# Kernel optimization log

Hardware: AMD Instinct MI355X
Metric: run time of the kernel (lower is better)

The kernel has to match this reference:

```python
import jax, jax.numpy as jnp
import numpy as np

D_MODEL = 1024
N_HEADS = 16
D_HEAD = D_MODEL // N_HEADS
IGNORE = -100000.0


def setup_inputs() -> dict:
    key = jax.random.key(0)
    ks = jax.random.split(key, 12)
    B, S = 4, 2048
    x_q = jax.random.normal(ks[0], (B, S, D_MODEL), dtype=jnp.float32)
    x_kv = jax.random.normal(ks[1], (B, S, D_MODEL), dtype=jnp.float32)
    # mask[q, k] == True means the score is replaced with IGNORE (masked out)
    mask = jax.random.randint(ks[2], (S, S), 0, 2) == 1
    sq = 1.0 / np.sqrt(D_MODEL)
    sh = 1.0 / np.sqrt(D_HEAD)
    W_Q = jax.random.normal(ks[3], (N_HEADS, D_MODEL, D_HEAD), dtype=jnp.float32) * sq
    W_K = jax.random.normal(ks[4], (N_HEADS, D_MODEL, D_HEAD), dtype=jnp.float32) * sq
    W_V = jax.random.normal(ks[5], (N_HEADS, D_MODEL, D_HEAD), dtype=jnp.float32) * sq
    W_O = jax.random.normal(ks[6], (N_HEADS, D_HEAD, D_MODEL), dtype=jnp.float32) * sh
    b_Q = jnp.zeros((N_HEADS, D_HEAD), dtype=jnp.float32)
    b_K = jnp.zeros((N_HEADS, D_HEAD), dtype=jnp.float32)
    b_V = jnp.zeros((N_HEADS, D_HEAD), dtype=jnp.float32)
    b_O = jnp.zeros((D_MODEL,), dtype=jnp.float32)
    return {"x_q": x_q, "x_kv": x_kv, "mask": mask,
            "W_Q": W_Q, "W_K": W_K, "W_V": W_V, "W_O": W_O,
            "b_Q": b_Q, "b_K": b_K, "b_V": b_V, "b_O": b_O}


def reference(x_q, x_kv, mask, W_Q, W_K, W_V, W_O, b_Q, b_K, b_V, b_O):
    # per-head QKV projections: b s d, n d h -> b s n h
    q = jnp.einsum('bsd,ndh->bsnh', x_q, W_Q) + b_Q
    k = jnp.einsum('bsd,ndh->bsnh', x_kv, W_K) + b_K
    v = jnp.einsum('bsd,ndh->bsnh', x_kv, W_V) + b_V
    scale = 1.0 / np.sqrt(D_HEAD)  # flex_attention default scaling
    # scores: [B, H, Sq, Sk]
    scores = jnp.einsum('bqnh,bknh->bnqk', q, k) * scale
    # score_mod: where mask True -> IGNORE
    scores = jnp.where(mask[None, None, :, :], jnp.float32(IGNORE), scores)
    attn = jax.nn.softmax(scores, axis=-1)
    z = jnp.einsum('bnqk,bknh->bqnh', attn, v)  # [B, Sq, H, Dh]
    # per-head output projection then sum over heads
    out = jnp.einsum('bqnh,nhd->bqd', z, W_O) + b_O
    return (out, z)
```

## Files before the change

kernel.cpp:

```cpp
#include <hip/hip_runtime.h>

#define S_LEN 2048
#define NHEAD 16
#define DHEAD 64
#define DMODEL 1024
#define BATCH 4
#define SC2 0.18033688011112042f

typedef short bf16x8 __attribute__((ext_vector_type(8)));
typedef float f32x4 __attribute__((ext_vector_type(4)));
typedef unsigned short u16;
typedef unsigned short u16x8 __attribute__((ext_vector_type(8)));
typedef unsigned short u16x4 __attribute__((ext_vector_type(4)));
typedef unsigned long long u64;
typedef unsigned long long u64x2 __attribute__((ext_vector_type(2)));

__device__ __forceinline__ u16 f2b(float f) {
  unsigned u = __builtin_bit_cast(unsigned, f);
  u += 0x7FFFu + ((u >> 16) & 1u);
  return (u16)(u >> 16);
}
__device__ __forceinline__ float b2f(u16 v) {
  unsigned u = ((unsigned)v) << 16;
  return __builtin_bit_cast(float, u);
}
__device__ __forceinline__ f32x4 mfma16(bf16x8 a, bf16x8 b, f32x4 c) {
  return __builtin_amdgcn_mfma_f32_16x16x32_bf16(a, b, c, 0, 0, 0);
}
__device__ __forceinline__ void load_lds16(const void* g, void* l) {
  __builtin_amdgcn_global_load_lds(
      (const __attribute__((address_space(1))) unsigned int*)g,
      (__attribute__((address_space(3))) unsigned int*)l, 16, 0, 0);
}
__device__ __forceinline__ void fexp2x4(float& a, float& b, float& c, float& d) {
  asm("v_exp_f32 %0, %0\n\t"
      "v_exp_f32 %1, %1\n\t"
      "v_exp_f32 %2, %2\n\t"
      "v_exp_f32 %3, %3\n\t"
      "s_nop 1"
      : "+v"(a), "+v"(b), "+v"(c), "+v"(d));
}
__device__ __forceinline__ unsigned cvtpk(float lo, float hi) {
  unsigned r;
  asm("v_cvt_pk_bf16_f32 %0, %1, %2" : "=v"(r) : "v"(lo), "v"(hi));
  return r;
}


__global__ void prepass(const float* __restrict__ xq, const float* __restrict__ xkv,
                        const int* __restrict__ M,
                        u16* __restrict__ XQ, u16* __restrict__ XKV,
                        u64* __restrict__ Mex)
{
  int i = blockIdx.x * 256 + threadIdx.x;
  int stride = gridDim.x * 256;
  for (; i < 5242880; i += stride) {
    if (i < 2097152) {
      float4 v = ((const float4*)xq)[i];
      u16x4 o = { f2b(v.x), f2b(v.y), f2b(v.z), f2b(v.w) };
      ((u16x4*)XQ)[i] = o;
    } else if (i < 4194304) {
      int j = i - 2097152;
      float4 v = ((const float4*)xkv)[j];
      u16x4 o = { f2b(v.x), f2b(v.y), f2b(v.z), f2b(v.w) };
      ((u16x4*)XKV)[j] = o;
    } else {
      int idx = i - 4194304;
      int q = idx >> 9, k = (idx & 511) * 4;
      int4 v = *(const int4*)(M + (size_t)q * S_LEN + k);
      int T = k >> 6, t = (k >> 4) & 3, g = (k >> 2) & 3;
      u64 m = 0;
      if (!v.x) m |= 0xFFFFull;
      if (!v.y) m |= 0xFFFF0000ull;
      if (!v.z) m |= 0xFFFF00000000ull;
      if (!v.w) m |= 0xFFFF000000000000ull;
      Mex[((size_t)q * 32 + T) * 16 + g * 4 + t] = m;
    }
  }
}

__global__ void repack4(const float* __restrict__ WQ, const float* __restrict__ WK,
                        const float* __restrict__ WV, const float* __restrict__ WO,
                        u16* __restrict__ WQT, u16* __restrict__ WKT,
                        u16* __restrict__ WVT, u16* __restrict__ WOH,
                        u16* __restrict__ WOL)
{
  const int which = blockIdx.z;
  const int tid = threadIdx.x;
  if (which < 3) {
    __shared__ u16 t[64][66];
    const float* W = which == 0 ? WQ : (which == 1 ? WK : WV);
    u16* WT = which == 0 ? WQT : (which == 1 ? WKT : WVT);
    const float scale = which == 0 ? SC2 : 1.0f;
    const int n = blockIdx.y, d0 = blockIdx.x * 64;
    const float* src = W + (size_t)n * 65536;
    for (int p = 0; p < 4; ++p) {
      int idx = p * 256 + tid;
      int r = idx >> 4, cs = idx & 15;
      float4 v = *(const float4*)(src + (size_t)(d0 + r) * 64 + cs * 4);
      t[r][cs*4+0] = f2b(v.x*scale); t[r][cs*4+1] = f2b(v.y*scale);
      t[r][cs*4+2] = f2b(v.z*scale); t[r][cs*4+3] = f2b(v.w*scale);
    }
    __syncthreads();
    for (int p = 0; p < 2; ++p) {
      int idx = p * 256 + tid;
      int hl = idx >> 3, ds = idx & 7;
      u16x8 o;
      for (int e = 0; e < 8; ++e) o[e] = t[ds*8+e][hl];
      *(u16x8*)(WT + (size_t)(n*64 + hl) * 1024 + d0 + ds*8) = o;
    }
  } else {
    __shared__ u16 th[64][66];
    __shared__ u16 tl[64][66];
    const int d0 = blockIdx.x * 64, c0 = blockIdx.y * 64;
    for (int p = 0; p < 4; ++p) {
      int idx = p * 256 + tid;
      int r = idx >> 4, cs = idx & 15;
      float4 v = *(const float4*)(WO + (size_t)(c0 + r) * 1024 + d0 + cs * 4);
      float f[4] = {v.x, v.y, v.z, v.w};
      for (int e = 0; e < 4; ++e) {
        u16 hb = f2b(f[e]);
        th[r][cs*4+e] = hb;
        tl[r][cs*4+e] = f2b(f[e] - b2f(hb));
      }
    }
    __syncthreads();
    for (int p = 0; p < 2; ++p) {
      int idx = p * 256 + tid;
      int dr = idx >> 3, cs = idx & 7;
      u16x8 oh, ol;
      for (int e = 0; e < 8; ++e) { oh[e] = th[cs*8+e][dr]; ol[e] = tl[cs*8+e][dr]; }
      *(u16x8*)(WOH + (size_t)(d0 + dr) * 1024 + c0 + cs*8) = oh;
      *(u16x8*)(WOL + (size_t)(d0 + dr) * 1024 + c0 + cs*8) = ol;
    }
  }
}


__global__ __launch_bounds__(256, 2)
void gemm_qkv(const u16* __restrict__ XQ, const u16* __restrict__ XKV,
              const u16* __restrict__ WQT, const u16* __restrict__ WKT,
              const u16* __restrict__ WVT,
              const float* __restrict__ bQ, const float* __restrict__ bK,
              const float* __restrict__ bV,
              u16* __restrict__ Qb, u16* __restrict__ Kb, u16* __restrict__ VT)
{
  const int which = blockIdx.z;
  const u16* A  = which == 0 ? XQ : XKV;
  const u16* Bt = which == 0 ? WQT : (which == 1 ? WKT : WVT);
  const float* bias = which == 0 ? bQ : (which == 1 ? bK : bV);
  const float bscale = which == 0 ? SC2 : 1.0f;

  __shared__ __align__(16) char As[16384];
  __shared__ __align__(16) char Bs[16384];
  const int tid = threadIdx.x, wid = tid >> 6, lane = tid & 63;
  const int lq = lane & 15, g = lane >> 4;
  const size_t am0 = (size_t)blockIdx.y * 128;
  const size_t bn0 = (size_t)blockIdx.x * 128;
  const int wr = (wid >> 1) * 64, wc = (wid & 1) * 64;
  f32x4 z4 = {0.f, 0.f, 0.f, 0.f};
  f32x4 acc[4][4];
  for (int i = 0; i < 4; ++i) for (int j = 0; j < 4; ++j) acc[i][j] = z4;
  for (int k0 = 0; k0 < DMODEL; k0 += 64) {
#pragma unroll
    for (int c = 0; c < 4; ++c) {
      int idx = c*256 + tid, r = idx >> 3, s = idx & 7;
      load_lds16(A + (am0 + r)*DMODEL + k0 + ((s ^ (r & 7)) << 3), As + idx*16);
    }
#pragma unroll
    for (int c = 0; c < 4; ++c) {
      int idx = c*256 + tid, r = idx >> 3, s = idx & 7;
      load_lds16(Bt + (bn0 + r)*DMODEL + k0 + ((s ^ (r & 7)) << 3), Bs + idx*16);
    }
    __syncthreads();
#pragma unroll
    for (int ks = 0; ks < 2; ++ks) {
      bf16x8 af[4], bfr[4];
#pragma unroll
      for (int i = 0; i < 4; ++i) {
        int row = wr + i*16 + lq;
        af[i] = *(const bf16x8*)(As + row*128 + (((ks*4 + g) ^ (row & 7)) << 4));
      }
#pragma unroll
      for (int j = 0; j < 4; ++j) {
        int row = wc + j*16 + lq;
        bfr[j] = *(const bf16x8*)(Bs + row*128 + (((ks*4 + g) ^ (row & 7)) << 4));
      }
#pragma unroll
      for (int i = 0; i < 4; ++i)
#pragma unroll
        for (int j = 0; j < 4; ++j)
          acc[i][j] = mfma16(af[i], bfr[j], acc[i][j]);
    }
    __syncthreads();
  }
  if (which < 2) {
    u16* Cout = which == 0 ? Qb : Kb;
#pragma unroll
    for (int i = 0; i < 4; ++i)
#pragma unroll
      for (int j = 0; j < 4; ++j) {
        size_t row = am0 + wr + i*16 + g*4;
        int col = (int)bn0 + wc + j*16 + lq;
        float bv = bias[col] * bscale;
#pragma unroll
        for (int r = 0; r < 4; ++r)
          Cout[(row + r)*DMODEL + col] = f2b(acc[i][j][r] + bv);
      }
  } else {
#pragma unroll
    for (int i = 0; i < 4; ++i)
#pragma unroll
      for (int j = 0; j < 4; ++j) {
        size_t row = am0 + wr + i*16 + g*4;
        int col = (int)bn0 + wc + j*16 + lq;
        float bv = bias[col];
        int bb = (int)(row >> 11), s = (int)(row & 2047);
        int hh2 = col >> 6, dh = col & 63;
        u16x4 o = { f2b(acc[i][j][0] + bv), f2b(acc[i][j][1] + bv),
                    f2b(acc[i][j][2] + bv), f2b(acc[i][j][3] + bv) };
        *(u16x4*)(VT + ((size_t)((bb*NHEAD + hh2)*DHEAD + dh))*S_LEN + s) = o;
      }
  }
}


__global__ __launch_bounds__(256, 2)
void gemm_out(const u16* __restrict__ Zh, const u16* __restrict__ Zl,
              const u16* __restrict__ Bh, const u16* __restrict__ Bl,
              const float* __restrict__ bias, float* __restrict__ Cout)
{
  __shared__ __align__(16) char Ah[16384];
  __shared__ __align__(16) char Al[16384];
  __shared__ __align__(16) char Bhs[16384];
  __shared__ __align__(16) char Bls[16384];
  const int tid = threadIdx.x, wid = tid >> 6, lane = tid & 63;
  const int lq = lane & 15, g = lane >> 4;
  const size_t am0 = (size_t)blockIdx.y * 128;
  const size_t bn0 = (size_t)blockIdx.x * 128;
  const int wr = (wid >> 1) * 64, wc = (wid & 1) * 64;
  f32x4 z4 = {0.f, 0.f, 0.f, 0.f};
  f32x4 acc[4][4];
  for (int i = 0; i < 4; ++i) for (int j = 0; j < 4; ++j) acc[i][j] = z4;
  for (int k0 = 0; k0 < DMODEL; k0 += 64) {
#pragma unroll
    for (int c = 0; c < 4; ++c) {
      int idx = c*256 + tid, r = idx >> 3, s = idx & 7;
      int so = (s ^ (r & 7)) << 3;
      load_lds16(Zh + (am0 + r)*DMODEL + k0 + so, Ah + idx*16);
      load_lds16(Zl + (am0 + r)*DMODEL + k0 + so, Al + idx*16);
      load_lds16(Bh + (bn0 + r)*DMODEL + k0 + so, Bhs + idx*16);
      load_lds16(Bl + (bn0 + r)*DMODEL + k0 + so, Bls + idx*16);
    }
    __syncthreads();
#pragma unroll
    for (int ks = 0; ks < 2; ++ks) {
      bf16x8 ah[4], al[4], bh4[4], bl4[4];
#pragma unroll
      for (int i = 0; i < 4; ++i) {
        int row = wr + i*16 + lq;
        int off = row*128 + (((ks*4 + g) ^ (row & 7)) << 4);
        ah[i] = *(const bf16x8*)(Ah + off);
        al[i] = *(const bf16x8*)(Al + off);
      }
#pragma unroll
      for (int j = 0; j < 4; ++j) {
        int row = wc + j*16 + lq;
        int off = row*128 + (((ks*4 + g) ^ (row & 7)) << 4);
        bh4[j] = *(const bf16x8*)(Bhs + off);
        bl4[j] = *(const bf16x8*)(Bls + off);
      }
#pragma unroll
      for (int i = 0; i < 4; ++i)
#pragma unroll
        for (int j = 0; j < 4; ++j) {
          acc[i][j] = mfma16(al[i], bh4[j], acc[i][j]);
          acc[i][j] = mfma16(ah[i], bl4[j], acc[i][j]);
          acc[i][j] = mfma16(ah[i], bh4[j], acc[i][j]);
        }
    }
    __syncthreads();
  }
#pragma unroll
  for (int i = 0; i < 4; ++i)
#pragma unroll
    for (int j = 0; j < 4; ++j) {
      size_t row = am0 + wr + i*16 + g*4;
      int col = (int)bn0 + wc + j*16 + lq;
      float bv = bias[col];
#pragma unroll
      for (int r = 0; r < 4; ++r)
        Cout[(row + r)*DMODEL + col] = acc[i][j][r] + bv;
    }
}

__global__ __launch_bounds__(256, 3)
void attn(const u16* __restrict__ Q, const u16* __restrict__ K,
          const u16* __restrict__ VT, const u64* __restrict__ Mex,
          float* __restrict__ Zf, u16* __restrict__ Zh, u16* __restrict__ Zl)
{
  __shared__ __align__(16) char L[49152];
  const int tid = threadIdx.x, wid = tid >> 6, lane = tid & 63;
  const int lq = lane & 15, g = lane >> 4;
  const int Lb = blockIdx.x;
  const int xcd = Lb & 7, slot = Lb >> 3;
  const int qt = slot & 15, pl = slot >> 4;
  const int pair = xcd * 8 + pl;
  const int h = pair & 15, b = pair >> 4;
  const int q0 = qt * 128;
  const int qw = q0 + wid * 32;

  bf16x8 qf[2][2];
#pragma unroll
  for (int u = 0; u < 2; ++u) {
    const u16* qp = Q + (size_t)(b*S_LEN + qw + u*16 + lq) * DMODEL + h*DHEAD + g*8;
    qf[u][0] = *(const bf16x8*)qp;
    qf[u][1] = *(const bf16x8*)(qp + 32);
  }
  bf16x8 ones;
#pragma unroll
  for (int e = 0; e < 8; ++e) ones[e] = (short)0x3F80;

  const f32x4 z4 = {0.f, 0.f, 0.f, 0.f};
  f32x4 Oc[2][4];
#pragma unroll
  for (int u = 0; u < 2; ++u)
#pragma unroll
    for (int t = 0; t < 4; ++t) Oc[u][t] = z4;
  f32x4 lrow[2] = {z4, z4};

  const u16* kp = K + (size_t)(b*S_LEN)*DMODEL + h*DHEAD;
  const u16* vp = VT + (size_t)((b*NHEAD + h)*DHEAD)*S_LEN;
  const u64* mx0 = Mex + (size_t)(qw + lq) * 512 + g*4;
  const u64* mx1 = Mex + (size_t)(qw + 16 + lq) * 512 + g*4;
  char* myP = L + 32768 + wid*4096;

  size_t ko[2], vo[2];
  int sd[2];
#pragma unroll
  for (int c = 0; c < 2; ++c) {
    int idx = c*256 + tid, r = idx >> 3, s = idx & 7, so = (s ^ (r & 7)) << 3;
    ko[c] = (size_t)r * DMODEL + so;
    vo[c] = (size_t)r * S_LEN + so;
    sd[c] = idx * 16;
  }

  bf16x8 kr0, kr1, vr0, vr1;
  kr0 = *(const bf16x8*)(kp + ko[0]); kr1 = *(const bf16x8*)(kp + ko[1]);
  vr0 = *(const bf16x8*)(vp + vo[0]); vr1 = *(const bf16x8*)(vp + vo[1]);
  u64x2 m0a = *(const u64x2*)(mx0), m0b = *(const u64x2*)(mx0 + 2);
  u64x2 m1a = *(const u64x2*)(mx1), m1b = *(const u64x2*)(mx1 + 2);
  kp += 64*DMODEL; vp += 64;
  *(bf16x8*)(L + sd[0]) = kr0;  *(bf16x8*)(L + sd[1]) = kr1;
  *(bf16x8*)(L + 8192 + sd[0]) = vr0;  *(bf16x8*)(L + 8192 + sd[1]) = vr1;
  __syncthreads();

  for (int it = 0; it < 32; ++it) {
    char* Bu = L + (it & 1) * 16384;
    char* Bn = L + ((it + 1) & 1) * 16384;
    u64x2 n0a = {0,0}, n0b = {0,0}, n1a = {0,0}, n1b = {0,0};
    if (it < 31) {
      kr0 = *(const bf16x8*)(kp + ko[0]); kr1 = *(const bf16x8*)(kp + ko[1]);
      vr0 = *(const bf16x8*)(vp + vo[0]); vr1 = *(const bf16x8*)(vp + vo[1]);
      n0a = *(const u64x2*)(mx0 + (it+1)*16);
      n0b = *(const u64x2*)(mx0 + (it+1)*16 + 2);
      n1a = *(const u64x2*)(mx1 + (it+1)*16);
      n1b = *(const u64x2*)(mx1 + (it+1)*16 + 2);
      kp += 64*DMODEL; vp += 64;
    }

    f32x4 st[2][4];
    __builtin_amdgcn_s_setprio(1);
#pragma unroll
    for (int t = 0; t < 4; ++t) {
      int row = t*16 + lq;
      bf16x8 kf0 = *(const bf16x8*)(Bu + row*128 + ((g ^ (row & 7)) << 4));
      bf16x8 kf1 = *(const bf16x8*)(Bu + row*128 + (((4 + g) ^ (row & 7)) << 4));
      st[0][t] = mfma16(kf1, qf[0][1], mfma16(kf0, qf[0][0], z4));
      st[1][t] = mfma16(kf1, qf[1][1], mfma16(kf0, qf[1][0], z4));
    }
    __builtin_amdgcn_s_setprio(0);

#pragma unroll
    for (int u = 0; u < 2; ++u) {
      char* pb = myP + (u*16 + lq) * 128;
#pragma unroll
      for (int t = 0; t < 4; ++t) {
        int sl = (((t*2 + (g >> 1)) ^ (lq & 7)) << 4) + ((g & 1) << 3);
        float p0 = st[u][t][0], p1 = st[u][t][1];
        float p2 = st[u][t][2], p3 = st[u][t][3];
        fexp2x4(p0, p1, p2, p3);
        u64 mt = u ? ((t < 2) ? m1a[t & 1] : m1b[t & 1])
                   : ((t < 2) ? m0a[t & 1] : m0b[t & 1]);
        union { unsigned w32[2]; u64 w64; } pw;
        pw.w32[0] = cvtpk(p0, p1);
        pw.w32[1] = cvtpk(p2, p3);
        *(u64*)(pb + sl) = pw.w64 & mt;
      }
    }
    asm volatile("s_waitcnt lgkmcnt(0)" ::: "memory");
    __builtin_amdgcn_sched_barrier(0);

    bf16x8 pf[2][2];
#pragma unroll
    for (int u = 0; u < 2; ++u) {
      char* pb = myP + (u*16 + lq) * 128;
      pf[u][0] = *(const bf16x8*)(pb + (((0 + g) ^ (lq & 7)) << 4));
      pf[u][1] = *(const bf16x8*)(pb + (((4 + g) ^ (lq & 7)) << 4));
    }

    __builtin_amdgcn_s_setprio(1);
    f32x4 ts0 = mfma16(pf[0][1], ones, mfma16(pf[0][0], ones, z4));
    f32x4 ts1 = mfma16(pf[1][1], ones, mfma16(pf[1][0], ones, z4));
#pragma unroll
    for (int t = 0; t < 4; ++t) {
      int row = t*16 + lq;
#pragma unroll
      for (int hh = 0; hh < 2; ++hh) {
        bf16x8 vf = *(const bf16x8*)(Bu + 8192 + row*128 + (((hh*4 + g) ^ (row & 7)) << 4));
        Oc[0][t] = mfma16(pf[0][hh], vf, Oc[0][t]);
        Oc[1][t] = mfma16(pf[1][hh], vf, Oc[1][t]);
      }
    }
    __builtin_amdgcn_s_setprio(0);
    lrow[0] += ts0;
    lrow[1] += ts1;

    if (it < 31) {
      *(bf16x8*)(Bn + sd[0]) = kr0;  *(bf16x8*)(Bn + sd[1]) = kr1;
      *(bf16x8*)(Bn + 8192 + sd[0]) = vr0;  *(bf16x8*)(Bn + 8192 + sd[1]) = vr1;
    }
    __syncthreads();
    m0a = n0a; m0b = n0b; m1a = n1a; m1b = n1b;
  }

#pragma unroll
  for (int u = 0; u < 2; ++u) {
    float i0 = 1.f / lrow[u][0], i1 = 1.f / lrow[u][1],
          i2 = 1.f / lrow[u][2], i3 = 1.f / lrow[u][3];
#pragma unroll
    for (int t = 0; t < 4; ++t) {
      size_t base = ((size_t)(b*S_LEN + qw + u*16 + g*4) * NHEAD + h) * DHEAD + t*16 + lq;
      float zv[4] = { Oc[u][t][0]*i0, Oc[u][t][1]*i1, Oc[u][t][2]*i2, Oc[u][t][3]*i3 };
#pragma unroll
      for (int r = 0; r < 4; ++r) {
        size_t off = base + (size_t)r * 1024;
        Zf[off] = zv[r];
        u16 hb = f2b(zv[r]);
        Zh[off] = hb;
        Zl[off] = f2b(zv[r] - b2f(hb));
      }
    }
  }
}


extern "C" void kernel_launch(void* const* d_in, const int* in_sizes, int n_in,
                              void* d_out, int out_size, void* d_ws, size_t ws_size,
                              hipStream_t stream) {
  const float* x_q  = (const float*)d_in[0];
  const float* x_kv = (const float*)d_in[1];
  const int*   mask = (const int*)d_in[2];
  const float* W_Q  = (const float*)d_in[3];
  const float* W_K  = (const float*)d_in[4];
  const float* W_V  = (const float*)d_in[5];
  const float* W_O  = (const float*)d_in[6];
  const float* b_Q  = (const float*)d_in[7];
  const float* b_K  = (const float*)d_in[8];
  const float* b_V  = (const float*)d_in[9];
  const float* b_O  = (const float*)d_in[10];

  if (ws_size < 102760448) return;

  u16* ws  = (u16*)d_ws;
  u16* XQ  = ws;
  u16* XKV = XQ  + 8388608;
  u16* WQT = XKV + 8388608;
  u16* WKT = WQT + 1048576;
  u16* WVT = WKT + 1048576;
  u16* WOH = WVT + 1048576;
  u16* WOL = WOH + 1048576;
  u16* Qb  = WOL + 1048576;
  u16* Kb  = Qb  + 8388608;
  u16* VTb = Kb  + 8388608;
  u64* Mxp = (u64*)(VTb + 8388608);
  u16* Zh  = XKV;
  u16* Zl  = XQ;

  float* out = (float*)d_out;
  float* zf  = out + 8388608;

  prepass<<<4096, 256, 0, stream>>>(x_q, x_kv, mask, XQ, XKV, Mxp);
  repack4<<<dim3(16,16,4), 256, 0, stream>>>(W_Q, W_K, W_V, W_O,
                                             WQT, WKT, WVT, WOH, WOL);
  gemm_qkv<<<dim3(8,64,3), 256, 0, stream>>>(XQ, XKV, WQT, WKT, WVT,
                                             b_Q, b_K, b_V, Qb, Kb, VTb);
  attn<<<1024, 256, 0, stream>>>(Qb, Kb, VTb, Mxp, zf, Zh, Zl);
  gemm_out<<<dim3(8,64), 256, 0, stream>>>(Zh, Zl, WOH, WOL, b_O, out);
}
```

Baseline: 250.6 us.

## Stage K/V tiles via direct global-to-LDS loads with manual vmcnt waits

Replaces the register-staged K/V prefetch (global load into VGPRs, then LDS store) with direct global-to-LDS loads issued into the next double-buffer slot. The __syncthreads calls become explicit s_waitcnt vmcnt plus s_barrier, with sched_barrier fences so the compiler cannot reorder across them. This is meant to save VGPRs and LDS-store instructions and to let the copies overlap compute. It relies on the hand-set vmcnt(8) count matching the number of outstanding loads, including the mask loads. If that count is wrong the kernel could read tiles before they have arrived.

```diff
diff --git a/kernel.cpp b/kernel.cpp
--- a/kernel.cpp
+++ b/kernel.cpp
@@ -345,29 +345,33 @@
     sd[c] = idx * 16;
   }
 
-  bf16x8 kr0, kr1, vr0, vr1;
-  kr0 = *(const bf16x8*)(kp + ko[0]); kr1 = *(const bf16x8*)(kp + ko[1]);
-  vr0 = *(const bf16x8*)(vp + vo[0]); vr1 = *(const bf16x8*)(vp + vo[1]);
+#define STAGE(Bb) do { \
+    load_lds16(kp + ko[0], (Bb) + sd[0]); \
+    load_lds16(kp + ko[1], (Bb) + sd[1]); \
+    load_lds16(vp + vo[0], (Bb) + 8192 + sd[0]); \
+    load_lds16(vp + vo[1], (Bb) + 8192 + sd[1]); \
+    kp += 64*DMODEL; vp += 64; \
+  } while (0)
+
+  STAGE(L);
   u64x2 m0a = *(const u64x2*)(mx0), m0b = *(const u64x2*)(mx0 + 2);
   u64x2 m1a = *(const u64x2*)(mx1), m1b = *(const u64x2*)(mx1 + 2);
-  kp += 64*DMODEL; vp += 64;
-  *(bf16x8*)(L + sd[0]) = kr0;  *(bf16x8*)(L + sd[1]) = kr1;
-  *(bf16x8*)(L + 8192 + sd[0]) = vr0;  *(bf16x8*)(L + 8192 + sd[1]) = vr1;
-  __syncthreads();
 
   for (int it = 0; it < 32; ++it) {
     char* Bu = L + (it & 1) * 16384;
-    char* Bn = L + ((it + 1) & 1) * 16384;
     u64x2 n0a = {0,0}, n0b = {0,0}, n1a = {0,0}, n1b = {0,0};
     if (it < 31) {
-      kr0 = *(const bf16x8*)(kp + ko[0]); kr1 = *(const bf16x8*)(kp + ko[1]);
-      vr0 = *(const bf16x8*)(vp + vo[0]); vr1 = *(const bf16x8*)(vp + vo[1]);
+      STAGE(L + ((it + 1) & 1) * 16384);
       n0a = *(const u64x2*)(mx0 + (it+1)*16);
       n0b = *(const u64x2*)(mx0 + (it+1)*16 + 2);
       n1a = *(const u64x2*)(mx1 + (it+1)*16);
       n1b = *(const u64x2*)(mx1 + (it+1)*16 + 2);
-      kp += 64*DMODEL; vp += 64;
-    }
+      asm volatile("s_waitcnt vmcnt(8)" ::: "memory");
+    } else {
+      asm volatile("s_waitcnt vmcnt(0)" ::: "memory");
+    }
+    __builtin_amdgcn_s_barrier();
+    __builtin_amdgcn_sched_barrier(0);
 
     f32x4 st[2][4];
     __builtin_amdgcn_s_setprio(1);
@@ -426,13 +430,11 @@
     lrow[0] += ts0;
     lrow[1] += ts1;
 
-    if (it < 31) {
-      *(bf16x8*)(Bn + sd[0]) = kr0;  *(bf16x8*)(Bn + sd[1]) = kr1;
-      *(bf16x8*)(Bn + 8192 + sd[0]) = vr0;  *(bf16x8*)(Bn + 8192 + sd[1]) = vr1;
-    }
-    __syncthreads();
+    __builtin_amdgcn_sched_barrier(0);
+    __builtin_amdgcn_s_barrier();
     m0a = n0a; m0b = n0b; m1a = n1a; m1b = n1b;
   }
+#undef STAGE
 
 #pragma unroll
   for (int u = 0; u < 2; ++u) {
```

Result: slower. 263.3 us (+5.1%).
